# Performance work log

Measured on AMD Instinct MI355X. Metric: run time of the kernel, lower is better.

Reference implementation:

```python
import jax, jax.numpy as jnp
import numpy as np

H = 256
L = 5
N = 50000


def setup_inputs() -> dict:
    key = jax.random.key(0)
    ks = jax.random.split(key, 12)
    E = 800000
    x = jax.random.normal(ks[0], (N, H), dtype=jnp.float32)
    edge_index = jax.random.randint(ks[1], (2, E), 0, N, dtype=jnp.int64)
    edge_weight = jax.random.uniform(ks[2], (E,), dtype=jnp.float32)
    s = 1.0 / np.sqrt(H)
    weight = jax.random.uniform(ks[3], (L, H, H), dtype=jnp.float32, minval=-s, maxval=s)
    w_ih = jax.random.uniform(ks[4], (3 * H, H), dtype=jnp.float32, minval=-s, maxval=s)
    w_hh = jax.random.uniform(ks[5], (3 * H, H), dtype=jnp.float32, minval=-s, maxval=s)
    b_ih = jax.random.uniform(ks[6], (3 * H,), dtype=jnp.float32, minval=-s, maxval=s)
    b_hh = jax.random.uniform(ks[7], (3 * H,), dtype=jnp.float32, minval=-s, maxval=s)
    fc_w = jax.random.uniform(ks[8], (1, H), dtype=jnp.float32, minval=-s, maxval=s)
    fc_b = jax.random.uniform(ks[9], (1,), dtype=jnp.float32, minval=-s, maxval=s)
    return {"x": x, "edge_index": edge_index, "edge_weight": edge_weight,
            "weight": weight, "w_ih": w_ih, "w_hh": w_hh, "b_ih": b_ih,
            "b_hh": b_hh, "fc_w": fc_w, "fc_b": fc_b, "prob": 0}


def _gru_cell(m, h, w_ih, w_hh, b_ih, b_hh):
    # PyTorch GRUCell: gates ordered (r, z, n)
    gi = m @ w_ih.T + b_ih  # [N, 3H]
    gh = h @ w_hh.T + b_hh  # [N, 3H]
    r = jax.nn.sigmoid(gi[:, :H] + gh[:, :H])
    z = jax.nn.sigmoid(gi[:, H:2 * H] + gh[:, H:2 * H])
    n = jnp.tanh(gi[:, 2 * H:] + r * gh[:, 2 * H:])
    return (1.0 - z) * n + z * h


def reference(x, edge_index, edge_weight, weight, w_ih, w_hh, b_ih, b_hh, fc_w, fc_b, prob):
    src = edge_index[0]
    dst = edge_index[1]
    h = x
    for i in range(L):
        m = h @ weight[i]                       # [N, H] per-layer linear transform
        msg = edge_weight[:, None] * m[src]     # [E, H] gather + edge weighting
        agg = jax.ops.segment_sum(msg, dst, num_segments=N)  # scatter-add
        h = _gru_cell(agg, h, w_ih, w_hh, b_ih, b_hh)
    h = jax.nn.relu(h)
    # dropout with p=prob; reference runs deterministically with p=0 (eval mode)
    out = h @ fc_w.T + fc_b                     # [N, 1]
    return out
```

## Files before the change

kernel.cpp:

```cpp
#include <hip/hip_runtime.h>
#include <hip/hip_bf16.h>
#include <math.h>


#define HDIM 256

using bf16x8 = __attribute__((ext_vector_type(8))) short;
using f32x4  = __attribute__((ext_vector_type(4))) float;

__device__ __forceinline__ bf16x8 ldfrag(const ushort* p) {
    union { uint4 u; bf16x8 f; } x;
    x.u = *(const uint4*)p;
    return x.f;
}
#define MFMA(a, b, c) __builtin_amdgcn_mfma_f32_16x16x32_bf16((a), (b), (c), 0, 0, 0)
#define GLD16(g, l)                                                            \
    __builtin_amdgcn_global_load_lds(                                          \
        (const __attribute__((address_space(1))) void*)(g),                    \
        (__attribute__((address_space(3))) void*)(l), 16, 0, 0)

__device__ __forceinline__ float ldf(const void* p, size_t i, int isbf) {
    if (isbf) return __bfloat162float(((const __hip_bfloat16*)p)[i]);
    return ((const float*)p)[i];
}
__device__ __forceinline__ ushort f2bs(float v) {
    __hip_bfloat16 b = __float2bfloat16(v);
    return *(ushort*)&b;
}
__device__ __forceinline__ float bs2f(ushort u) {
    __hip_bfloat16 b = *(__hip_bfloat16*)&u;
    return __bfloat162float(b);
}
__device__ __forceinline__ size_t taddrH(int n, int k) {
    return (size_t)(n >> 4) * 4096 + (size_t)((k >> 5) << 9)
         + (size_t)(((k >> 3) & 3) << 7) + (size_t)((n & 15) << 3) + (k & 7);
}
__device__ __forceinline__ size_t taddrA(int n, int k) {
    return (size_t)(n >> 4) * 8192 + (size_t)((k >> 5) << 9)
         + (size_t)(((k >> 3) & 3) << 7) + (size_t)((n & 15) << 3) + (k & 7);
}

__global__ void detect_k(const void* x, const void* ei, int* flags) {
    if (blockIdx.x == 0 && threadIdx.x == 0) {
        const __hip_bfloat16* xb = (const __hip_bfloat16*)x;
        int isbf = 1;
        for (int i = 0; i < 1024; ++i) {
            float v = fabsf(__bfloat162float(xb[i]));
            if (!(v < 1e6f)) { isbf = 0; break; }
        }
        flags[0] = isbf;
        const int* e32 = (const int*)ei;
        int orv = e32[1] | e32[3] | e32[5] | e32[7] | e32[9] | e32[11];
        flags[1] = (orv == 0) ? 1 : 0;
    }
}

__global__ void conv_h0_k(const void* x, ushort* HH, ushort* HL, ushort* hB,
                          const int* flags, int useHL, int Nn, size_t npad256) {
    size_t i = (size_t)blockIdx.x * blockDim.x + threadIdx.x;
    if (i >= npad256) return;
    const int n = (int)(i >> 8), k = (int)(i & 255);
    float v = 0.f;
    if (n < Nn) v = ldf(x, i, flags[0]);
    const ushort hi = f2bs(v);
    const ushort lo = f2bs(v - bs2f(hi));
    const size_t a = taddrH(n, k);
    HH[a] = hi;
    if (useHL) HL[a] = lo;
    hB[(size_t)n * 512 + k] = hi;
    hB[(size_t)n * 512 + 256 + k] = lo;
}

__global__ void repack_k(const ushort* __restrict__ TH, const ushort* __restrict__ TL,
                         ushort* __restrict__ hB, int useHL, int ngroups) {
    const int g = blockIdx.x * 256 + threadIdx.x;
    if (g >= ngroups) return;
    const int t = g >> 9, o = (g & 511) * 8;
    const int k = ((o >> 9) << 5) | (((o >> 7) & 3) << 3);
    const int n = t * 16 + ((o >> 3) & 15);
    const uint4 hv = *(const uint4*)&TH[(size_t)t * 4096 + o];
    *(uint4*)&hB[(size_t)n * 512 + k] = hv;
    uint4 lv;
    if (useHL) lv = *(const uint4*)&TL[(size_t)t * 4096 + o];
    else       lv = make_uint4(0u, 0u, 0u, 0u);
    *(uint4*)&hB[(size_t)n * 512 + 256 + k] = lv;
}

__global__ __launch_bounds__(256)
void prep1_k(const void* wih, const void* w, float* wihp, const int* flags) {
    __shared__ float As[16][260], Bs[16][260];
    const int bx = blockIdx.x;
    const int l = bx / 768, rem = bx % 768;
    const int rt = (rem >> 4) << 4, kt = (rem & 15) << 4;
    const int tid = threadIdx.x, isbf = flags[0];
    for (int idx = tid; idx < 4096; idx += 256) {
        const int row = idx >> 8, col = idx & 255;
        As[row][col] = ldf(wih, (size_t)(rt + row) * 256 + col, isbf);
        Bs[row][col] = ldf(w, (size_t)l * 65536 + (size_t)(kt + row) * 256 + col, isbf);
    }
    __syncthreads();
    const int ri = tid >> 4, ki = tid & 15;
    float acc = 0.f;
    for (int j = 0; j < 256; ++j) acc = fmaf(As[ri][j], Bs[ki][j], acc);
    wihp[((size_t)l * 768 + rt + ri) * 256 + kt + ki] = acc;
}

__global__ void prep2_k(const float* __restrict__ wihp, const void* whh,
                        const void* bih, const void* bhh,
                        ushort* BgAH, ushort* BgAL, ushort* BgBH, ushort* BgBL,
                        float* bsum, float* bni, float* bnh,
                        const int* flags, int L) {
    const int i = blockIdx.x * blockDim.x + threadIdx.x;
    const int isbf = flags[0];
    if (i < (L << 19)) {
        const int l = i >> 19, r2 = i & 524287;
        const int j = r2 >> 9, k = r2 & 511;
        const int g = (j >> 4) & 3, b = ((j >> 6) << 4) + (j & 15);
        const int kk = k & 255;
        const float v = (g == 3) ? 0.f
                      : wihp[((size_t)l * 768 + g * 256 + b) * 256 + kk];
        const ushort hi = f2bs(v);
        const int ct = j >> 4, c = k >> 5;
        const size_t a = (size_t)l * 524288 + (size_t)(ct * 16 + c) * 512
                       + (size_t)(((k >> 3) & 3) << 7) + ((j & 15) << 3) + (k & 7);
        BgAH[a] = hi; BgAL[a] = f2bs(v - bs2f(hi));
    }
    if (i < 524288) {
        const int j = i >> 9, k = i & 511;
        const int g = (j >> 4) & 3, b = ((j >> 6) << 4) + (j & 15);
        const int kk = k & 255;
        float v;
        if (g == 0)      v = ldf(whh, (size_t)b * 256 + kk, isbf);
        else if (g == 1) v = ldf(whh, (size_t)(256 + b) * 256 + kk, isbf);
        else if (g == 2) v = 0.f;
        else             v = ldf(whh, (size_t)(512 + b) * 256 + kk, isbf);
        const ushort hi = f2bs(v);
        const int ct = j >> 4, c = k >> 5;
        const size_t a = (size_t)(ct * 16 + c) * 512
                       + (size_t)(((k >> 3) & 3) << 7) + ((j & 15) << 3) + (k & 7);
        BgBH[a] = hi; BgBL[a] = f2bs(v - bs2f(hi));
    }
    if (i < 512) bsum[i] = ldf(bih, i, isbf) + ldf(bhh, i, isbf);
    if (i < 256) {
        bni[i] = ldf(bih, 512 + i, isbf);
        bnh[i] = ldf(bhh, 512 + i, isbf);
    }
}


__global__ void zero_int_k(int* p, int n) {
    int i = blockIdx.x * blockDim.x + threadIdx.x;
    if (i < n) p[i] = 0;
}

__global__ void count_k(const void* ei, int* cnt, const int* flags, int E) {
    int e = blockIdx.x * blockDim.x + threadIdx.x;
    if (e >= E) return;
    const int* e32 = (const int*)ei;
    int d = flags[1] ? e32[2 * ((size_t)E + e)] : e32[(size_t)E + e];
    atomicAdd(&cnt[d], 1);
}

__global__ __launch_bounds__(256)
void scan1_k(const int* cnt, int* ptr, int* bsumN, int N) {
    __shared__ int s[256];
    const int t = threadIdx.x;
    const int gid = blockIdx.x * 256 + t;
    int v = (gid < N) ? cnt[gid] : 0;
    const int own = v;
    s[t] = v;
    __syncthreads();
#pragma unroll
    for (int off = 1; off < 256; off <<= 1) {
        int add = (t >= off) ? s[t - off] : 0;
        __syncthreads();
        s[t] += add;
        __syncthreads();
    }
    if (gid < N) ptr[gid] = s[t] - own;
    if (t == 255) bsumN[blockIdx.x] = s[255];
}

__global__ __launch_bounds__(256)
void scan2_k(int* bsumN, int NB) {
    __shared__ int s[256];
    __shared__ int carry;
    const int t = threadIdx.x;
    if (t == 0) carry = 0;
    __syncthreads();
    for (int base = 0; base < NB; base += 256) {
        const int i = base + t;
        int v = (i < NB) ? bsumN[i] : 0;
        const int own = v;
        s[t] = v;
        __syncthreads();
#pragma unroll
        for (int off = 1; off < 256; off <<= 1) {
            int add = (t >= off) ? s[t - off] : 0;
            __syncthreads();
            s[t] += add;
            __syncthreads();
        }
        if (i < NB) bsumN[i] = carry + s[t] - own;
        __syncthreads();
        if (t == 0) carry += s[255];
        __syncthreads();
    }
}

__global__ void scan3_k(int* ptr, int* cursor, const int* bsumN, int N, int E) {
    const int gid = blockIdx.x * 256 + threadIdx.x;
    if (gid < N) {
        const int p = ptr[gid] + bsumN[blockIdx.x];
        ptr[gid] = p;
        cursor[gid] = p;
    }
    if (gid == 0) ptr[N] = E;
}

__global__ void fill_k(const void* ei, const void* ew, int* cursor,
                       int* srcs, float* wse, const int* flags, int E) {
    int e = blockIdx.x * blockDim.x + threadIdx.x;
    if (e >= E) return;
    const int* e32 = (const int*)ei;
    int s, d;
    if (flags[1]) { s = e32[2 * (size_t)e]; d = e32[2 * ((size_t)E + e)]; }
    else          { s = e32[e];             d = e32[(size_t)E + e]; }
    const int p = atomicAdd(&cursor[d], 1);
    srcs[p] = s;
    wse[p] = ldf(ew, e, flags[0]);
}

__global__ __launch_bounds__(256)
void spmm_k(const ushort* __restrict__ hB, const int* __restrict__ ptr,
            const int* __restrict__ srcs, const float* __restrict__ wse,
            ushort* __restrict__ AGG, int N) {
    const int node = blockIdx.x * 4 + (threadIdx.x >> 6);
    if (node >= N) return;
    const int lane = threadIdx.x & 63;
    const int p0 = ptr[node], p1 = ptr[node + 1];
    float av[8];
#pragma unroll
    for (int i = 0; i < 8; ++i) av[i] = 0.f;
    union U8 { ushort u[8]; uint4 v; };
    int j = p0;
    for (; j + 1 < p1; j += 2) {
        const int s0 = srcs[j], s1 = srcs[j + 1];
        const float w0 = wse[j], w1 = wse[j + 1];
        U8 u0, u1;
        u0.v = *(const uint4*)&hB[(size_t)s0 * 512 + lane * 8];
        u1.v = *(const uint4*)&hB[(size_t)s1 * 512 + lane * 8];
#pragma unroll
        for (int i = 0; i < 8; ++i) av[i] = fmaf(w0, bs2f(u0.u[i]), av[i]);
#pragma unroll
        for (int i = 0; i < 8; ++i) av[i] = fmaf(w1, bs2f(u1.u[i]), av[i]);
    }
    if (j < p1) {
        const int s0 = srcs[j];
        const float w0 = wse[j];
        U8 u0;
        u0.v = *(const uint4*)&hB[(size_t)s0 * 512 + lane * 8];
#pragma unroll
        for (int i = 0; i < 8; ++i) av[i] = fmaf(w0, bs2f(u0.u[i]), av[i]);
    }
#pragma unroll
    for (int i = 0; i < 8; ++i) av[i] += __shfl_xor(av[i], 32);
    if (lane < 32) {
        const int k0 = lane * 8;
        union U8 hi8, lo8;
#pragma unroll
        for (int i = 0; i < 8; ++i) {
            const ushort hi = f2bs(av[i]);
            hi8.u[i] = hi;
            lo8.u[i] = f2bs(av[i] - bs2f(hi));
        }
        *(uint4*)&AGG[taddrA(node, k0)] = hi8.v;
        *(uint4*)&AGG[taddrA(node, 256 + k0)] = lo8.v;
    }
}

__global__ __launch_bounds__(256)
void gates_k(const ushort* __restrict__ AGG,
             const ushort* __restrict__ HH, const ushort* __restrict__ HL,
             const ushort* __restrict__ BgAH, const ushort* __restrict__ BgAL,
             const ushort* __restrict__ BgBH, const ushort* __restrict__ BgBL,
             const float* __restrict__ bsum, const float* __restrict__ bni,
             const float* __restrict__ bnh,
             ushort* __restrict__ HnH, ushort* __restrict__ HnL,
             const int* __restrict__ flags, int useHL, int nRB) {
    __shared__ ushort lds[24576];
    const int x = blockIdx.x & 7, rem = blockIdx.x >> 3;
    const int cgB = rem & 7, rbHi = rem >> 3;
    const int rb = rbHi * 8 + x;
    if (rb >= nRB) return;
    const int tid = threadIdx.x, lane = tid & 63;
    const int wv = __builtin_amdgcn_readfirstlane(tid >> 6);
    const int wr = wv & 1, wc = wv >> 1;
    const int lm = lane & 15, lq = lane >> 4;
    const int fullsplit = !flags[0];
    const int rt = rb * 8, t0 = 2 * wv;
    f32x4 acc[4][4];
#pragma unroll
    for (int i = 0; i < 4; ++i)
#pragma unroll
        for (int j = 0; j < 4; ++j) acc[i][j] = (f32x4){0.f, 0.f, 0.f, 0.f};

#define GT_STEP(BH, BL, c0l, A0, ASTRIDE, JSKIP, DOLO)                         \
    do {                                                                       \
        __syncthreads();                                                       \
        GLD16((A0) + (size_t)lane * 8, &lds[t0 * 512]);                        \
        GLD16((A0) + (ASTRIDE) + (size_t)lane * 8, &lds[t0 * 512 + 512]);      \
        GLD16((A0) + 512 + (size_t)lane * 8, &lds[12288 + t0 * 512]);          \
        GLD16((A0) + (ASTRIDE) + 512 + (size_t)lane * 8, &lds[12288 + t0 * 512 + 512]); \
        const size_t bb = ((size_t)(8 * cgB + t0) * 16 + (size_t)(c0l)) * 512; \
        if ((t0 & 3) != (JSKIP)) {                                             \
            GLD16((BH) + bb + (size_t)lane * 8, &lds[4096 + t0 * 512]);        \
            GLD16((BH) + bb + 512 + (size_t)lane * 8, &lds[12288 + 4096 + t0 * 512]); \
        }                                                                      \
        if (((t0 + 1) & 3) != (JSKIP)) {                                       \
            GLD16((BH) + bb + 8192 + (size_t)lane * 8, &lds[4096 + t0 * 512 + 512]); \
            GLD16((BH) + bb + 8704 + (size_t)lane * 8, &lds[12288 + 4096 + t0 * 512 + 512]); \
        }                                                                      \
        if (DOLO) {                                                            \
            if ((t0 & 3) != (JSKIP)) {                                         \
                GLD16((BL) + bb + (size_t)lane * 8, &lds[8192 + t0 * 512]);    \
                GLD16((BL) + bb + 512 + (size_t)lane * 8, &lds[12288 + 8192 + t0 * 512]); \
            }                                                                  \
            if (((t0 + 1) & 3) != (JSKIP)) {                                   \
                GLD16((BL) + bb + 8192 + (size_t)lane * 8, &lds[8192 + t0 * 512 + 512]); \
                GLD16((BL) + bb + 8704 + (size_t)lane * 8, &lds[12288 + 8192 + t0 * 512 + 512]); \
            }                                                                  \
        }                                                                      \
        __syncthreads();                                                       \
        _Pragma("unroll")                                                      \
        for (int sb = 0; sb < 2; ++sb) {                                       \
            const int lb = sb * 12288;                                         \
            bf16x8 af[4];                                                      \
            _Pragma("unroll")                                                  \
            for (int i = 0; i < 4; ++i)                                        \
                af[i] = ldfrag(&lds[lb + (4 * wr + i) * 512 + lq * 128 + lm * 8]); \
            _Pragma("unroll")                                                  \
            for (int j = 0; j < 4; ++j) {                                      \
                if (j == (JSKIP)) continue;                                    \
                const bf16x8 bj = ldfrag(&lds[lb + 4096 + (4 * wc + j) * 512 + lq * 128 + lm * 8]); \
                _Pragma("unroll")                                              \
                for (int i = 0; i < 4; ++i) acc[i][j] = MFMA(af[i], bj, acc[i][j]); \
            }                                                                  \
            if (DOLO) {                                                        \
                _Pragma("unroll")                                              \
                for (int j = 0; j < 4; ++j) {                                  \
                    if (j == (JSKIP)) continue;                                \
                    const bf16x8 bl = ldfrag(&lds[lb + 8192 + (4 * wc + j) * 512 + lq * 128 + lm * 8]); \
                    _Pragma("unroll")                                          \
                    for (int i = 0; i < 4; ++i) acc[i][j] = MFMA(af[i], bl, acc[i][j]); \
                }                                                              \
            }                                                                  \
        }                                                                      \
    } while (0)

    for (int s = 0; s < 4; ++s) {
        const ushort* a0 = AGG + (size_t)(rt + t0) * 8192 + (size_t)(2 * s) * 512;
        GT_STEP(BgAH, BgAL, 2 * s, a0, 8192, 3, fullsplit);
    }
    for (int s = 4; s < 8; ++s) {
        const ushort* a0 = AGG + (size_t)(rt + t0) * 8192 + (size_t)(2 * s) * 512;
        GT_STEP(BgAH, BgAL, 2 * s, a0, 8192, 3, 0);
    }
    for (int s = 8; s < 12; ++s) {
        const ushort* a0 = HH + (size_t)(rt + t0) * 4096 + (size_t)(2 * s - 16) * 512;
        GT_STEP(BgBH, BgBL, 2 * s - 16, a0, 4096, 2, fullsplit);
    }
    if (useHL) {
        for (int s = 12; s < 16; ++s) {
            const ushort* a0 = HL + (size_t)(rt + t0) * 4096 + (size_t)(2 * s - 24) * 512;
            GT_STEP(BgBH, BgBL, 2 * s - 16, a0, 4096, 2, 0);
        }
    }
#undef GT_STEP

    const int b = (2 * cgB + wc) * 16 + lm;
    const float rbias = bsum[b], zbias = bsum[256 + b];
    const float ibias = bni[b], hbias = bnh[b];
#pragma unroll
    for (int i = 0; i < 4; ++i) {
        const int row0 = rb * 128 + wr * 64 + i * 16 + lq * 4;
#pragma unroll
        for (int v = 0; v < 4; ++v) {
            const int row = row0 + v;
            const size_t ho = taddrH(row, b);
            float hold = bs2f(HH[ho]);
            if (useHL) hold += bs2f(HL[ho]);
            const float r = 1.f / (1.f + expf(-(acc[i][0][v] + rbias)));
            const float z = 1.f / (1.f + expf(-(acc[i][1][v] + zbias)));
            const float nn = tanhf(acc[i][2][v] + ibias + r * (acc[i][3][v] + hbias));
            const float hv = (1.f - z) * nn + z * hold;
            const ushort hi = f2bs(hv);
            HnH[ho] = hi;
            if (useHL) HnL[ho] = f2bs(hv - bs2f(hi));
        }
    }
}

__global__ void final_k(const ushort* __restrict__ HH, const ushort* __restrict__ HL,
                        const void* fcw, const void* fcb,
                        void* out, const int* flags, int useHL, int N) {
    const int n = blockIdx.x;
    const int t = threadIdx.x;
    const int isbf = flags[0];
    const size_t off = taddrH(n, t);
    float h = bs2f(HH[off]);
    if (useHL) h += bs2f(HL[off]);
    float v = fmaxf(h, 0.f) * ldf(fcw, t, isbf);
#pragma unroll
    for (int offx = 32; offx >= 1; offx >>= 1) v += __shfl_down(v, offx);
    __shared__ float red[4];
    if ((t & 63) == 0) red[t >> 6] = v;
    __syncthreads();
    if (t == 0) {
        const float s = red[0] + red[1] + red[2] + red[3] + ldf(fcb, 0, isbf);
        if (isbf) ((__hip_bfloat16*)out)[n] = __float2bfloat16(s);
        else      ((float*)out)[n] = s;
    }
}

extern "C" void kernel_launch(void* const* d_in, const int* in_sizes, int n_in,
                              void* d_out, int out_size, void* d_ws, size_t ws_size,
                              hipStream_t stream) {
    const int H = HDIM;
    const int N = in_sizes[0] / H;
    const int E = in_sizes[2];
    const int L = in_sizes[3] / (H * H);
    const int NB = (N + 255) / 256;
    const int nRB = (N + 127) / 128;
    const size_t NPAD = (size_t)nRB * 128;
    const size_t hHalf = NPAD * 256;
    const size_t aggHalf = NPAD * 512;

    char* p = (char*)d_ws;
    int*    flags = (int*)p;              p += 64;
    ushort* AGG  = (ushort*)p;            p += aggHalf * 2;
    ushort* HxH  = (ushort*)p;            p += hHalf * 2;
    ushort* HyH  = (ushort*)p;            p += hHalf * 2;
    ushort* hB   = (ushort*)p;            p += NPAD * 512 * 2;
    float*  wihp = (float*)p;             p += (size_t)L * 768 * 256 * 4;
    ushort* BgAH = (ushort*)p;            p += (size_t)L * 524288 * 2;
    ushort* BgAL = (ushort*)p;            p += (size_t)L * 524288 * 2;
    ushort* BgBH = (ushort*)p;            p += (size_t)524288 * 2;
    ushort* BgBL = (ushort*)p;            p += (size_t)524288 * 2;
    float*  bsum = (float*)p;             p += 512 * 4;
    float*  bni  = (float*)p;             p += 256 * 4;
    float*  bnh  = (float*)p;             p += 256 * 4;
    int*    ptr  = (int*)p;               p += (size_t)(N + 1) * 4;
    int*    cursor = (int*)p;             p += (size_t)N * 4;
    int*    bsumN  = (int*)p;             p += (size_t)NB * 4;
    int*    srcs   = (int*)p;             p += (size_t)E * 4;
    float*  wse    = (float*)p;           p += (size_t)E * 4;
    const size_t need_reduced = (size_t)(p - (char*)d_ws);
    ushort* HxL = (ushort*)p;
    ushort* HyL = (ushort*)(p + hHalf * 2);
    const size_t need_full = need_reduced + 2 * hHalf * 2;
    const int useHL = (ws_size >= need_full) ? 1 : 0;
    if (!useHL) { HxL = HxH; HyL = HyH; }

    detect_k<<<dim3(1), dim3(64), 0, stream>>>(d_in[0], d_in[1], flags);
    conv_h0_k<<<dim3((unsigned)NPAD), dim3(256), 0, stream>>>(
        d_in[0], HxH, HxL, hB, flags, useHL, N, NPAD * 256);
    prep1_k<<<dim3((unsigned)(L * 768)), dim3(256), 0, stream>>>(
        d_in[4], d_in[3], wihp, flags);
    prep2_k<<<dim3((unsigned)(L * 2048)), dim3(256), 0, stream>>>(
        wihp, d_in[5], d_in[6], d_in[7],
        BgAH, BgAL, BgBH, BgBL, bsum, bni, bnh, flags, L);

    zero_int_k<<<dim3(NB), dim3(256), 0, stream>>>(cursor, N);
    count_k<<<dim3((E + 255) / 256), dim3(256), 0, stream>>>(d_in[1], cursor, flags, E);
    scan1_k<<<dim3(NB), dim3(256), 0, stream>>>(cursor, ptr, bsumN, N);
    scan2_k<<<dim3(1), dim3(256), 0, stream>>>(bsumN, NB);
    scan3_k<<<dim3(NB), dim3(256), 0, stream>>>(ptr, cursor, bsumN, N, E);
    fill_k<<<dim3((E + 255) / 256), dim3(256), 0, stream>>>(
        d_in[1], d_in[2], cursor, srcs, wse, flags, E);

    const dim3 blk(256);
    const unsigned gGrid = 64u * (unsigned)((nRB + 7) / 8);
    const int ngroups = (int)(NPAD * 32);
    const unsigned rGrid = (unsigned)((ngroups + 255) / 256);
    ushort *HcH = HxH, *HcL = HxL, *HnH = HyH, *HnL = HyL;
    for (int l = 0; l < L; ++l) {
        spmm_k<<<dim3((N + 3) / 4), blk, 0, stream>>>(hB, ptr, srcs, wse, AGG, N);
        gates_k<<<dim3(gGrid), blk, 0, stream>>>(
            AGG, HcH, HcL,
            BgAH + (size_t)l * 524288, BgAL + (size_t)l * 524288,
            BgBH, BgBL, bsum, bni, bnh, HnH, HnL, flags, useHL, nRB);
        if (l + 1 < L)
            repack_k<<<dim3(rGrid), blk, 0, stream>>>(HnH, HnL, hB, useHL, ngroups);
        ushort* t;
        t = HcH; HcH = HnH; HnH = t;
        t = HcL; HcL = HnL; HnL = t;
    }
    final_k<<<dim3(N), blk, 0, stream>>>(
        HcH, HcL, d_in[8], d_in[9], d_out, flags, useHL, N);
}
```

Baseline: 1.962 ms.

## Add triple-buffered async LDS pipeline for GRU gate GEMM in full-split mode

```diff
diff --git a/kernel.cpp b/kernel.cpp
--- a/kernel.cpp
+++ b/kernel.cpp
@@ -18,6 +18,11 @@
     __builtin_amdgcn_global_load_lds(                                          \
         (const __attribute__((address_space(1))) void*)(g),                    \
         (__attribute__((address_space(3))) void*)(l), 16, 0, 0)
+#define VMW8() asm volatile("s_waitcnt vmcnt(8)" ::: "memory")
+#define VMW4() asm volatile("s_waitcnt vmcnt(4)" ::: "memory")
+#define VMW0() asm volatile("s_waitcnt vmcnt(0)" ::: "memory")
+#define LGW()  asm volatile("s_waitcnt lgkmcnt(0)" ::: "memory")
+#define SBAR() __builtin_amdgcn_s_barrier()
 
 __device__ __forceinline__ float ldf(const void* p, size_t i, int isbf) {
     if (isbf) return __bfloat162float(((const __hip_bfloat16*)p)[i]);
@@ -305,6 +310,69 @@
 #pragma unroll
         for (int j = 0; j < 4; ++j) acc[i][j] = (f32x4){0.f, 0.f, 0.f, 0.f};
 
+    if (fullsplit && useHL) {
+        auto stage = [&](int xx, int sl3) {
+            const ushort* a0;
+            size_t astride;
+            if (xx < 24) {
+                const int ck = (xx < 16) ? (xx & 7) : (xx - 8);
+                a0 = AGG + (size_t)(rt + t0) * 8192 + (size_t)ck * 512;
+                astride = 8192;
+            } else {
+                const ushort* hp = (xx < 40) ? HH : HL;
+                const int ck = (xx < 40) ? ((xx - 24) & 7) : (xx - 40);
+                a0 = hp + (size_t)(rt + t0) * 4096 + (size_t)ck * 512;
+                astride = 4096;
+            }
+            const ushort* B;
+            int cl;
+            if (xx < 8)       { B = BgAH; cl = xx; }
+            else if (xx < 16) { B = BgAL; cl = xx - 8; }
+            else if (xx < 24) { B = BgAH; cl = xx - 8; }
+            else if (xx < 32) { B = BgBH; cl = xx - 24; }
+            else if (xx < 40) { B = BgBL; cl = xx - 32; }
+            else              { B = BgBH; cl = xx - 32; }
+            const size_t bb = ((size_t)(8 * cgB + t0) * 16 + (size_t)cl) * 512;
+            ushort* sl = &lds[sl3 * 8192];
+            GLD16(a0 + (size_t)lane * 8, sl + t0 * 512);
+            GLD16(a0 + astride + (size_t)lane * 8, sl + t0 * 512 + 512);
+            GLD16(B + bb + (size_t)lane * 8, sl + 4096 + t0 * 512);
+            GLD16(B + bb + 8192 + (size_t)lane * 8, sl + 4096 + t0 * 512 + 512);
+        };
+        stage(0, 0); stage(1, 1); stage(2, 2);
+        VMW8();
+        SBAR();
+#pragma unroll
+        for (int c = 0; c < 48; ++c) {
+            const ushort* sl = &lds[(c % 3) * 8192];
+            const size_t boff = (size_t)lq * 128 + (size_t)lm * 8;
+            bf16x8 af[4];
+#pragma unroll
+            for (int i = 0; i < 4; ++i)
+                af[i] = ldfrag(sl + (4 * wr + i) * 512 + boff);
+            const bf16x8 bf0 = ldfrag(sl + 4096 + (4 * wc + 0) * 512 + boff);
+            const bf16x8 bf1 = ldfrag(sl + 4096 + (4 * wc + 1) * 512 + boff);
+            const bf16x8 bf2 = ldfrag(sl + 4096 + (4 * wc + ((c < 24) ? 2 : 3)) * 512 + boff);
+            LGW();
+            if (c < 46) { VMW4(); }
+            else        { VMW0(); }
+            SBAR();
+            if (c + 3 < 48) stage(c + 3, (c + 3) % 3);
+            __builtin_amdgcn_s_setprio(1);
+#pragma unroll
+            for (int i = 0; i < 4; ++i) acc[i][0] = MFMA(af[i], bf0, acc[i][0]);
+#pragma unroll
+            for (int i = 0; i < 4; ++i) acc[i][1] = MFMA(af[i], bf1, acc[i][1]);
+            if (c < 24) {
+#pragma unroll
+                for (int i = 0; i < 4; ++i) acc[i][2] = MFMA(af[i], bf2, acc[i][2]);
+            } else {
+#pragma unroll
+                for (int i = 0; i < 4; ++i) acc[i][3] = MFMA(af[i], bf2, acc[i][3]);
+            }
+            __builtin_amdgcn_s_setprio(0);
+        }
+    } else {
 #define GT_STEP(BH, BL, c0l, A0, ASTRIDE, JSKIP, DOLO)                         \
     do {                                                                       \
         __syncthreads();                                                       \
@@ -357,26 +425,27 @@
             }                                                                  \
         }                                                                      \
     } while (0)
-
-    for (int s = 0; s < 4; ++s) {
-        const ushort* a0 = AGG + (size_t)(rt + t0) * 8192 + (size_t)(2 * s) * 512;
-        GT_STEP(BgAH, BgAL, 2 * s, a0, 8192, 3, fullsplit);
-    }
-    for (int s = 4; s < 8; ++s) {
-        const ushort* a0 = AGG + (size_t)(rt + t0) * 8192 + (size_t)(2 * s) * 512;
-        GT_STEP(BgAH, BgAL, 2 * s, a0, 8192, 3, 0);
-    }
-    for (int s = 8; s < 12; ++s) {
-        const ushort* a0 = HH + (size_t)(rt + t0) * 4096 + (size_t)(2 * s - 16) * 512;
-        GT_STEP(BgBH, BgBL, 2 * s - 16, a0, 4096, 2, fullsplit);
-    }
-    if (useHL) {
-        for (int s = 12; s < 16; ++s) {
-            const ushort* a0 = HL + (size_t)(rt + t0) * 4096 + (size_t)(2 * s - 24) * 512;
-            GT_STEP(BgBH, BgBL, 2 * s - 16, a0, 4096, 2, 0);
-        }
-    }
+        for (int s = 0; s < 4; ++s) {
+            const ushort* a0 = AGG + (size_t)(rt + t0) * 8192 + (size_t)(2 * s) * 512;
+            GT_STEP(BgAH, BgAL, 2 * s, a0, 8192, 3, fullsplit);
+        }
+        for (int s = 4; s < 8; ++s) {
+            const ushort* a0 = AGG + (size_t)(rt + t0) * 8192 + (size_t)(2 * s) * 512;
+            GT_STEP(BgAH, BgAL, 2 * s, a0, 8192, 3, 0);
+        }
+        for (int s = 8; s < 12; ++s) {
+            const ushort* a0 = HH + (size_t)(rt + t0) * 4096 + (size_t)(2 * s - 16) * 512;
+            GT_STEP(BgBH, BgBL, 2 * s - 16, a0, 4096, 2, fullsplit);
+        }
+        if (useHL) {
+            for (int s = 12; s < 16; ++s) {
+                const ushort* a0 = HL + (size_t)(rt + t0) * 4096 + (size_t)(2 * s - 24) * 512;
+                GT_STEP(BgBH, BgBL, 2 * s - 16, a0, 4096, 2, 0);
+            }
+        }
 #undef GT_STEP
+        __syncthreads();
+    }
 
     const int b = (2 * cgB + wc) * 16 + lm;
     const float rbias = bsum[b], zbias = bsum[256 + b];
```

Measured after the change: 2.057 ms. +4.8%, slower.
